# Performance work log

Measured on AMD Instinct MI355X. Metric: run time of the kernel, lower is better.

Reference implementation:

```python
import jax, jax.numpy as jnp
import numpy as np

D_MODEL = 1024
NUM_HEADS = 16
HEAD_DIM = D_MODEL // NUM_HEADS
B, S = 4, 2048


def setup_inputs() -> dict:
    key = jax.random.key(0)
    ks = jax.random.split(key, 12)
    s = 1.0 / np.sqrt(D_MODEL)
    return {
        "inputs_q": jax.random.normal(ks[0], (B, S, D_MODEL), jnp.float32),
        "inputs_k": jax.random.normal(ks[1], (B, S, D_MODEL), jnp.float32),
        "inputs_v": jax.random.normal(ks[2], (B, S, D_MODEL), jnp.float32),
        "Wq": jax.random.normal(ks[3], (D_MODEL, D_MODEL), jnp.float32) * s,
        "bq": jax.random.normal(ks[4], (D_MODEL,), jnp.float32) * 0.01,
        "Wk": jax.random.normal(ks[5], (D_MODEL, D_MODEL), jnp.float32) * s,
        "bk": jax.random.normal(ks[6], (D_MODEL,), jnp.float32) * 0.01,
        "Wv": jax.random.normal(ks[7], (D_MODEL, D_MODEL), jnp.float32) * s,
        "bv": jax.random.normal(ks[8], (D_MODEL,), jnp.float32) * 0.01,
        "Wo": jax.random.normal(ks[9], (D_MODEL, D_MODEL), jnp.float32) * s,
        "bo": jax.random.normal(ks[10], (D_MODEL,), jnp.float32) * 0.01,
    }


def reference(inputs_q, inputs_k, inputs_v, Wq, bq, Wk, bk, Wv, bv, Wo, bo):
    b, s, _ = inputs_q.shape
    # linear projections
    q = inputs_q @ Wq + bq  # [b, s, d_model]
    k = inputs_k @ Wk + bk
    v = inputs_v @ Wv + bv
    # split heads: bsd -> bhsd
    q = q.reshape(b, s, NUM_HEADS, HEAD_DIM).transpose(0, 2, 1, 3)
    k = k.reshape(b, s, NUM_HEADS, HEAD_DIM).transpose(0, 2, 1, 3)
    v = v.reshape(b, s, NUM_HEADS, HEAD_DIM).transpose(0, 2, 1, 3)
    scale = 1.0 / jnp.sqrt(jnp.asarray(HEAD_DIM, q.dtype))
    scores = jnp.einsum('bhqd,bhkd->bhqk', q, k) * scale  # [b,h,s,s]
    # causal mask: position q attends to k <= q
    causal = jnp.tril(jnp.ones((s, s), dtype=bool))
    scores = jnp.where(causal[None, None], scores, jnp.asarray(-jnp.inf, scores.dtype))
    attn = jax.nn.softmax(scores, axis=-1)
    ctx = jnp.einsum('bhqk,bhkd->bhqd', attn, v)  # [b,h,s,hd]
    ctx = ctx.transpose(0, 2, 1, 3).reshape(b, s, D_MODEL)
    return ctx @ Wo + bo
```

## Files before the change

kernel.cpp:

```cpp
#include <hip/hip_runtime.h>
#include <math.h>
#include <type_traits>

typedef __bf16 bf16;
typedef __attribute__((ext_vector_type(8))) __bf16 bf16x8;
typedef __attribute__((ext_vector_type(4))) float f32x4;
typedef __attribute__((ext_vector_type(16))) float f32x16;

#define SEQ 2048
#define DM 1024
#define NH 16
#define HD 64
#define BATCH 4

#define NEG_BIG (-1e30f)
#define SCALE_L2E 0.18033688011f

__device__ inline bf16x8 cvt_f32x8(const float* p) {
  f32x4 x0 = *(const f32x4*)p;
  f32x4 x1 = *(const f32x4*)(p + 4);
  bf16x8 r;
  r[0] = (bf16)x0[0]; r[1] = (bf16)x0[1]; r[2] = (bf16)x0[2]; r[3] = (bf16)x0[3];
  r[4] = (bf16)x1[0]; r[5] = (bf16)x1[1]; r[6] = (bf16)x1[2]; r[7] = (bf16)x1[3];
  return r;
}

__device__ inline void async_copy16(const bf16* g, bf16* l) {
  __builtin_amdgcn_global_load_lds(
      (const __attribute__((address_space(1))) unsigned int*)g,
      (__attribute__((address_space(3))) unsigned int*)l, 16, 0, 0);
}

__global__ __launch_bounds__(256) void cvt_kernel(const float* __restrict__ src,
                                                  bf16* __restrict__ dst) {
  size_t i = ((size_t)blockIdx.x * 256 + threadIdx.x) * 8;
  *(bf16x8*)(dst + i) = cvt_f32x8(src + i);
}

__global__ __launch_bounds__(256) void transpose_w_kernel(
    const float* __restrict__ Wq, const float* __restrict__ Wk,
    const float* __restrict__ Wv, const float* __restrict__ Wo,
    bf16* __restrict__ Tq, bf16* __restrict__ Tk,
    bf16* __restrict__ Tv, bf16* __restrict__ To) {
  __shared__ bf16 tile[64 * 66];
  int z = blockIdx.z;
  const float* src = (z == 0) ? Wq : (z == 1) ? Wk : (z == 2) ? Wv : Wo;
  bf16* dst = (z == 0) ? Tq : (z == 1) ? Tk : (z == 2) ? Tv : To;
  int n0 = blockIdx.x * 64, k0 = blockIdx.y * 64;
  int t = threadIdx.x;
  int c = t & 63, rr = t >> 6;
#pragma unroll
  for (int i = 0; i < 16; i++) {
    int k = i * 4 + rr;
    tile[k * 66 + c] = (bf16)src[(size_t)(k0 + k) * DM + n0 + c];
  }
  __syncthreads();
#pragma unroll
  for (int i = 0; i < 16; i++) {
    int n = i * 4 + rr;
    dst[(size_t)(n0 + n) * DM + k0 + c] = tile[c * 66 + n];
  }
}

template <typename CT, int MODE>
__global__ __launch_bounds__(256) void gemm_bias_kernel(
    const bf16* __restrict__ A, const bf16* __restrict__ Bt,
    const float* __restrict__ bias, CT* __restrict__ C) {
  __shared__ bf16 As[2][128 * 32];
  __shared__ bf16 Bs[2][128 * 32];
  int m0 = blockIdx.x * 128, n0 = blockIdx.y * 128;
  int t = threadIdx.x;
  int wave = t >> 6, lane = t & 63, lr = lane & 15, lq = lane >> 4;
  int wm = (wave & 1) * 64, wn = (wave >> 1) * 64;

  f32x4 acc[4][4];
#pragma unroll
  for (int i = 0; i < 4; i++)
#pragma unroll
    for (int j = 0; j < 4; j++) acc[i][j] = (f32x4){0.f, 0.f, 0.f, 0.f};

  int srow = wave * 32 + (lane >> 2);
  int skc = lane & 3;
  const bf16* gA0 = A + (size_t)(m0 + srow) * DM + skc * 8;
  const bf16* gA1 = gA0 + (size_t)16 * DM;
  const bf16* gB0 = Bt + (size_t)(n0 + srow) * DM + skc * 8;
  const bf16* gB1 = gB0 + (size_t)16 * DM;
  int oA0 = (wave * 128) * 8;
  int oA1 = (wave * 128 + 64) * 8;

  auto stage = [&](int buf) {
    async_copy16(gA0, &As[buf][oA0]);
    async_copy16(gA1, &As[buf][oA1]);
    async_copy16(gB0, &Bs[buf][oA0]);
    async_copy16(gB1, &Bs[buf][oA1]);
    gA0 += 32; gA1 += 32; gB0 += 32; gB1 += 32;
  };

  stage(0);
  __syncthreads();
  int cur = 0;
  for (int k0 = 0; k0 < DM; k0 += 32) {
    if (k0 + 32 < DM) stage(cur ^ 1);

    bf16x8 af[4], bfr[4];
#pragma unroll
    for (int i = 0; i < 4; i++)
      af[i] = *(const bf16x8*)&As[cur][(wm + i * 16 + lr) * 32 + lq * 8];
#pragma unroll
    for (int j = 0; j < 4; j++)
      bfr[j] = *(const bf16x8*)&Bs[cur][(wn + j * 16 + lr) * 32 + lq * 8];
    __builtin_amdgcn_s_setprio(1);
#pragma unroll
    for (int i = 0; i < 4; i++)
#pragma unroll
      for (int j = 0; j < 4; j++)
        acc[i][j] = __builtin_amdgcn_mfma_f32_16x16x32_bf16(af[i], bfr[j],
                                                            acc[i][j], 0, 0, 0);
    __builtin_amdgcn_s_setprio(0);
    __syncthreads();
    cur ^= 1;
  }

#pragma unroll
  for (int j = 0; j < 4; j++) {
    int col = n0 + wn + j * 16 + lr;
    float bv = bias[col];
#pragma unroll
    for (int i = 0; i < 4; i++) {
      int row0 = m0 + wm + i * 16 + lq * 4;
#pragma unroll
      for (int r = 0; r < 4; r++) {
        int row = row0 + r;
        float v = acc[i][j][r] + bv;
        if constexpr (MODE == 0) {
          C[(size_t)row * DM + col] = (CT)v;
        } else if constexpr (MODE == 1) {
          int b = row >> 11, s = row & 2047, h = col >> 6, d = col & 63;
          C[((size_t)(b * NH + h) * SEQ + s) * HD + d] = (CT)v;
        } else {
          int b = row >> 11, s = row & 2047, h = col >> 6, d = col & 63;
          C[((size_t)(b * NH + h) * HD + d) * SEQ + s] = (CT)v;
        }
      }
    }
  }
}

__global__ __launch_bounds__(256, 2) void attention_kernel(
    const bf16* __restrict__ Qc, const bf16* __restrict__ Kc,
    const bf16* __restrict__ Vt, bf16* __restrict__ ctx) {
  int t = threadIdx.x, wave = t >> 6, lane = t & 63;
  int l31 = lane & 31, hh = lane >> 5;

  int bid = blockIdx.x;
  int xcd = bid & 7, qq = bid >> 3;
  int g = xcd + 8 * (qq & 7);
  int bx = qq >> 3;
  int h = g & 15, b = g >> 4;
  int p = bx * 4 + wave;

  const bf16* Qb = Qc + (size_t)(b * NH + h) * SEQ * HD;
  const bf16* Kb = Kc + (size_t)(b * NH + h) * SEQ * HD;
  const bf16* Vb = Vt + (size_t)(b * NH + h) * HD * SEQ;
  bf16* Cb = ctx + (size_t)b * SEQ * DM + h * HD;

#pragma unroll 1
  for (int pass = 0; pass < 2; pass++) {
    int tq = pass ? (63 - p) : p;
    int q0 = tq * 32;

    bf16x8 qf[4];
#pragma unroll
    for (int st = 0; st < 4; st++)
      qf[st] = *(const bf16x8*)&Qb[(size_t)(q0 + l31) * HD + st * 16 + hh * 8];

    f32x16 o[2];
#pragma unroll
    for (int dt = 0; dt < 2; dt++)
#pragma unroll
      for (int r = 0; r < 16; r++) o[dt][r] = 0.f;
    float m_st = NEG_BIG, l_st = 0.f;

    int nch = (tq >> 1) + 1;
#pragma unroll 1
    for (int c = 0; c < nch; c++) {
      int kv0 = c * 64;
      bf16x8 kf[2][4];
#pragma unroll
      for (int kt = 0; kt < 2; kt++)
#pragma unroll
        for (int st = 0; st < 4; st++)
          kf[kt][st] = *(const bf16x8*)&Kb[(size_t)(kv0 + kt * 32 + l31) * HD +
                                           st * 16 + hh * 8];
      bf16x8 vf[2][4];
#pragma unroll
      for (int dt = 0; dt < 2; dt++)
#pragma unroll
        for (int ks = 0; ks < 4; ks++)
          vf[dt][ks] = *(const bf16x8*)&Vb[(size_t)(dt * 32 + l31) * SEQ + kv0 +
                                           ks * 16 + hh * 8];

      f32x16 s[2];
      __builtin_amdgcn_s_setprio(1);
#pragma unroll
      for (int kt = 0; kt < 2; kt++) {
        f32x16 acc;
#pragma unroll
        for (int r = 0; r < 16; r++) acc[r] = 0.f;
#pragma unroll
        for (int st = 0; st < 4; st++)
          acc = __builtin_amdgcn_mfma_f32_32x32x16_bf16(kf[kt][st], qf[st],
                                                        acc, 0, 0, 0);
        s[kt] = acc;
      }
      __builtin_amdgcn_s_setprio(0);

      bool diag = (c == nch - 1);
      if (diag) {
        int q_g = q0 + l31;
#pragma unroll
        for (int kt = 0; kt < 2; kt++)
#pragma unroll
          for (int r = 0; r < 16; r++) {
            int key = kv0 + kt * 32 + (r & 3) + 8 * (r >> 2) + 4 * hh;
            float v = s[kt][r] * SCALE_L2E;
            s[kt][r] = (key > q_g) ? NEG_BIG : v;
          }
      } else {
#pragma unroll
        for (int kt = 0; kt < 2; kt++)
#pragma unroll
          for (int r = 0; r < 16; r++) s[kt][r] *= SCALE_L2E;
      }

      float mx = s[0][0];
#pragma unroll
      for (int r = 1; r < 16; r++) mx = fmaxf(mx, s[0][r]);
#pragma unroll
      for (int r = 0; r < 16; r++) mx = fmaxf(mx, s[1][r]);
      mx = fmaxf(mx, __shfl_xor(mx, 32));
      float mnew = fmaxf(m_st, mx);
      float alpha = exp2f(m_st - mnew);
      m_st = mnew;
      float rs = 0.f;
#pragma unroll
      for (int kt = 0; kt < 2; kt++)
#pragma unroll
        for (int r = 0; r < 16; r++) {
          float pv = exp2f(s[kt][r] - mnew);
          s[kt][r] = pv;
          rs += pv;
        }
      rs += __shfl_xor(rs, 32);
      l_st = l_st * alpha + rs;
#pragma unroll
      for (int dt = 0; dt < 2; dt++)
#pragma unroll
        for (int r = 0; r < 16; r++) o[dt][r] *= alpha;

      unsigned int W[2][8];
#pragma unroll
      for (int kt = 0; kt < 2; kt++)
#pragma unroll
        for (int w = 0; w < 8; w++) {
          unsigned int u;
          asm("v_cvt_pk_bf16_f32 %0, %1, %2"
              : "=v"(u)
              : "v"(s[kt][2 * w]), "v"(s[kt][2 * w + 1]));
          W[kt][w] = u;
        }
      bf16x8 pf[4];
#pragma unroll
      for (int kt = 0; kt < 2; kt++) {
        unsigned int x1 = hh ? W[kt][0] : W[kt][2];
        unsigned int x2 = hh ? W[kt][1] : W[kt][3];
        unsigned int x3 = hh ? W[kt][4] : W[kt][6];
        unsigned int x4 = hh ? W[kt][5] : W[kt][7];
        unsigned int y1 = (unsigned int)__shfl_xor((int)x1, 32);
        unsigned int y2 = (unsigned int)__shfl_xor((int)x2, 32);
        unsigned int y3 = (unsigned int)__shfl_xor((int)x3, 32);
        unsigned int y4 = (unsigned int)__shfl_xor((int)x4, 32);
        unsigned int* f0 = (unsigned int*)&pf[2 * kt];
        unsigned int* f1 = (unsigned int*)&pf[2 * kt + 1];
        f0[0] = hh ? y1 : W[kt][0];
        f0[1] = hh ? y2 : W[kt][1];
        f0[2] = hh ? W[kt][2] : y1;
        f0[3] = hh ? W[kt][3] : y2;
        f1[0] = hh ? y3 : W[kt][4];
        f1[1] = hh ? y4 : W[kt][5];
        f1[2] = hh ? W[kt][6] : y3;
        f1[3] = hh ? W[kt][7] : y4;
      }

      __builtin_amdgcn_s_setprio(1);
#pragma unroll
      for (int dt = 0; dt < 2; dt++)
#pragma unroll
        for (int ks = 0; ks < 4; ks++)
          o[dt] = __builtin_amdgcn_mfma_f32_32x32x16_bf16(vf[dt][ks], pf[ks],
                                                          o[dt], 0, 0, 0);
      __builtin_amdgcn_s_setprio(0);
    }

    float inv = 1.f / l_st;
    int row = q0 + l31;
#pragma unroll
    for (int dt = 0; dt < 2; dt++)
#pragma unroll
      for (int r = 0; r < 16; r += 2) {
        float va = o[dt][r] * inv;
        float vb = o[dt][r + 1] * inv;
        unsigned int u;
        asm("v_cvt_pk_bf16_f32 %0, %1, %2" : "=v"(u) : "v"(va), "v"(vb));
        int d = dt * 32 + (r & 3) + 8 * (r >> 2) + 4 * hh;
        *(unsigned int*)&Cb[(size_t)row * DM + d] = u;
      }
  }
}

extern "C" void kernel_launch(void* const* d_in, const int* in_sizes, int n_in,
                              void* d_out, int out_size, void* d_ws,
                              size_t ws_size, hipStream_t stream) {
  const float* iq = (const float*)d_in[0];
  const float* ik = (const float*)d_in[1];
  const float* iv = (const float*)d_in[2];
  const float* Wq = (const float*)d_in[3];
  const float* bq = (const float*)d_in[4];
  const float* Wk = (const float*)d_in[5];
  const float* bk = (const float*)d_in[6];
  const float* Wv = (const float*)d_in[7];
  const float* bv = (const float*)d_in[8];
  const float* Wo = (const float*)d_in[9];
  const float* bo = (const float*)d_in[10];

  char* ws = (char*)d_ws;
  const size_t MB = 1024 * 1024;
  bf16* Tq = (bf16*)(ws + 0 * MB);
  bf16* Tk = (bf16*)(ws + 2 * MB);
  bf16* Tv = (bf16*)(ws + 4 * MB);
  bf16* To = (bf16*)(ws + 6 * MB);
  bf16* Qc = (bf16*)(ws + 8 * MB);
  bf16* Kc = (bf16*)(ws + 24 * MB);
  bf16* X = (bf16*)(ws + 40 * MB);
  bf16* Vtp = (bf16*)d_out;
  bf16* Cx = (bf16*)(ws + 40 * MB);

  transpose_w_kernel<<<dim3(16, 16, 4), 256, 0, stream>>>(Wq, Wk, Wv, Wo, Tq,
                                                          Tk, Tv, To);
  cvt_kernel<<<dim3(4096), 256, 0, stream>>>(iq, X);
  gemm_bias_kernel<bf16, 1><<<dim3(64, 8), 256, 0, stream>>>(X, Tq, bq, Qc);
  cvt_kernel<<<dim3(4096), 256, 0, stream>>>(ik, X);
  gemm_bias_kernel<bf16, 1><<<dim3(64, 8), 256, 0, stream>>>(X, Tk, bk, Kc);
  cvt_kernel<<<dim3(4096), 256, 0, stream>>>(iv, X);
  gemm_bias_kernel<bf16, 2><<<dim3(64, 8), 256, 0, stream>>>(X, Tv, bv, Vtp);
  attention_kernel<<<dim3(512), 256, 0, stream>>>(Qc, Kc, Vtp, Cx);
  gemm_bias_kernel<float, 0><<<dim3(64, 8), 256, 0, stream>>>(Cx, To, bo,
                                                              (float*)d_out);
}
```

Baseline: 395.6 us.

## Fuse fp32-to-bf16 input conversion into batched QKV projection GEMM

Removes the three separate conversion kernels and instead loads fp32 activations straight into registers inside the GEMM, converting to bf16 before writing to shared memory. The three Q/K/V projections are batched into one launch using a z grid dimension. This is meant to cut the extra global round-trip of the bf16 copy, remove five launches, and give more blocks per launch to fill the GPU. The trade-off is that A-tile loads become synchronous register loads doubled in bytes rather than async LDS copies, which adds register pressure and latency to hide.

```diff
diff --git a/kernel.cpp b/kernel.cpp
--- a/kernel.cpp
+++ b/kernel.cpp
@@ -16,9 +16,7 @@
 #define NEG_BIG (-1e30f)
 #define SCALE_L2E 0.18033688011f
 
-__device__ inline bf16x8 cvt_f32x8(const float* p) {
-  f32x4 x0 = *(const f32x4*)p;
-  f32x4 x1 = *(const f32x4*)(p + 4);
+__device__ inline bf16x8 pack_bf16x8(f32x4 x0, f32x4 x1) {
   bf16x8 r;
   r[0] = (bf16)x0[0]; r[1] = (bf16)x0[1]; r[2] = (bf16)x0[2]; r[3] = (bf16)x0[3];
   r[4] = (bf16)x1[0]; r[5] = (bf16)x1[1]; r[6] = (bf16)x1[2]; r[7] = (bf16)x1[3];
@@ -29,12 +27,6 @@
   __builtin_amdgcn_global_load_lds(
       (const __attribute__((address_space(1))) unsigned int*)g,
       (__attribute__((address_space(3))) unsigned int*)l, 16, 0, 0);
-}
-
-__global__ __launch_bounds__(256) void cvt_kernel(const float* __restrict__ src,
-                                                  bf16* __restrict__ dst) {
-  size_t i = ((size_t)blockIdx.x * 256 + threadIdx.x) * 8;
-  *(bf16x8*)(dst + i) = cvt_f32x8(src + i);
 }
 
 __global__ __launch_bounds__(256) void transpose_w_kernel(
@@ -62,6 +54,117 @@
   }
 }
 
+__global__ __launch_bounds__(256) void qkv_gemm_kernel(
+    const float* __restrict__ Aq, const float* __restrict__ Ak,
+    const float* __restrict__ Av, const bf16* __restrict__ Tq,
+    const bf16* __restrict__ Tk, const bf16* __restrict__ Tv,
+    const float* __restrict__ bq, const float* __restrict__ bk,
+    const float* __restrict__ bv, bf16* __restrict__ Cq,
+    bf16* __restrict__ Ck, bf16* __restrict__ Cv) {
+  int z = blockIdx.z;
+  const float* A = (z == 0) ? Aq : (z == 1) ? Ak : Av;
+  const bf16* Bt = (z == 0) ? Tq : (z == 1) ? Tk : Tv;
+  const float* bias = (z == 0) ? bq : (z == 1) ? bk : bv;
+  bf16* C = (z == 0) ? Cq : (z == 1) ? Ck : Cv;
+
+  __shared__ bf16 As[2][128 * 32];
+  __shared__ bf16 Bs[2][128 * 32];
+  int m0 = blockIdx.x * 128, n0 = blockIdx.y * 128;
+  int t = threadIdx.x;
+  int wave = t >> 6, lane = t & 63, lr = lane & 15, lq = lane >> 4;
+  int wm = (wave & 1) * 64, wn = (wave >> 1) * 64;
+
+  f32x4 acc[4][4];
+#pragma unroll
+  for (int i = 0; i < 4; i++)
+#pragma unroll
+    for (int j = 0; j < 4; j++) acc[i][j] = (f32x4){0.f, 0.f, 0.f, 0.f};
+
+  int arow = t >> 2;
+  int acolf = (t & 3) * 8;
+  const float* gA = A + (size_t)(m0 + arow) * DM + acolf;
+  const float* gA2 = gA + (size_t)64 * DM;
+  f32x4 ar[2][2];
+
+  auto loadA = [&](int k0) {
+    ar[0][0] = *(const f32x4*)(gA + k0);
+    ar[0][1] = *(const f32x4*)(gA + k0 + 4);
+    ar[1][0] = *(const f32x4*)(gA2 + k0);
+    ar[1][1] = *(const f32x4*)(gA2 + k0 + 4);
+  };
+  auto cvtwriteA = [&](int buf) {
+    *(bf16x8*)&As[buf][arow * 32 + acolf] = pack_bf16x8(ar[0][0], ar[0][1]);
+    *(bf16x8*)&As[buf][(arow + 64) * 32 + acolf] =
+        pack_bf16x8(ar[1][0], ar[1][1]);
+  };
+
+  int srow = wave * 32 + (lane >> 2);
+  int skc = lane & 3;
+  const bf16* gB0 = Bt + (size_t)(n0 + srow) * DM + skc * 8;
+  const bf16* gB1 = gB0 + (size_t)16 * DM;
+  int oB0 = (wave * 128) * 8;
+  int oB1 = (wave * 128 + 64) * 8;
+  auto stageB = [&](int buf) {
+    async_copy16(gB0, &Bs[buf][oB0]);
+    async_copy16(gB1, &Bs[buf][oB1]);
+    gB0 += 32; gB1 += 32;
+  };
+
+  loadA(0);
+  stageB(0);
+  cvtwriteA(0);
+  __syncthreads();
+
+  int cur = 0;
+  for (int k0 = 0; k0 < DM; k0 += 32) {
+    bool more = (k0 + 32 < DM);
+    if (more) {
+      loadA(k0 + 32);
+      stageB(cur ^ 1);
+    }
+
+    bf16x8 af[4], bfr[4];
+#pragma unroll
+    for (int i = 0; i < 4; i++)
+      af[i] = *(const bf16x8*)&As[cur][(wm + i * 16 + lr) * 32 + lq * 8];
+#pragma unroll
+    for (int j = 0; j < 4; j++)
+      bfr[j] = *(const bf16x8*)&Bs[cur][(wn + j * 16 + lr) * 32 + lq * 8];
+    __builtin_amdgcn_s_setprio(1);
+#pragma unroll
+    for (int i = 0; i < 4; i++)
+#pragma unroll
+      for (int j = 0; j < 4; j++)
+        acc[i][j] = __builtin_amdgcn_mfma_f32_16x16x32_bf16(af[i], bfr[j],
+                                                            acc[i][j], 0, 0, 0);
+    __builtin_amdgcn_s_setprio(0);
+    if (more) cvtwriteA(cur ^ 1);
+    __syncthreads();
+    cur ^= 1;
+  }
+
+#pragma unroll
+  for (int j = 0; j < 4; j++) {
+    int col = n0 + wn + j * 16 + lr;
+    float bv2 = bias[col];
+#pragma unroll
+    for (int i = 0; i < 4; i++) {
+      int row0 = m0 + wm + i * 16 + lq * 4;
+#pragma unroll
+      for (int r = 0; r < 4; r++) {
+        int row = row0 + r;
+        float v = acc[i][j][r] + bv2;
+        int b = row >> 11, s = row & 2047, h = col >> 6, d = col & 63;
+        if (z < 2) {
+          C[((size_t)(b * NH + h) * SEQ + s) * HD + d] = (bf16)v;
+        } else {
+          C[((size_t)(b * NH + h) * HD + d) * SEQ + s] = (bf16)v;
+        }
+      }
+    }
+  }
+}
+
 template <typename CT, int MODE>
 __global__ __launch_bounds__(256) void gemm_bias_kernel(
     const bf16* __restrict__ A, const bf16* __restrict__ Bt,
@@ -134,12 +237,9 @@
         float v = acc[i][j][r] + bv;
         if constexpr (MODE == 0) {
           C[(size_t)row * DM + col] = (CT)v;
-        } else if constexpr (MODE == 1) {
+        } else {
           int b = row >> 11, s = row & 2047, h = col >> 6, d = col & 63;
           C[((size_t)(b * NH + h) * SEQ + s) * HD + d] = (CT)v;
-        } else {
-          int b = row >> 11, s = row & 2047, h = col >> 6, d = col & 63;
-          C[((size_t)(b * NH + h) * HD + d) * SEQ + s] = (CT)v;
         }
       }
     }
@@ -341,18 +441,13 @@
   bf16* To = (bf16*)(ws + 6 * MB);
   bf16* Qc = (bf16*)(ws + 8 * MB);
   bf16* Kc = (bf16*)(ws + 24 * MB);
-  bf16* X = (bf16*)(ws + 40 * MB);
+  bf16* Cx = (bf16*)(ws + 40 * MB);
   bf16* Vtp = (bf16*)d_out;
-  bf16* Cx = (bf16*)(ws + 40 * MB);
 
   transpose_w_kernel<<<dim3(16, 16, 4), 256, 0, stream>>>(Wq, Wk, Wv, Wo, Tq,
                                                           Tk, Tv, To);
-  cvt_kernel<<<dim3(4096), 256, 0, stream>>>(iq, X);
-  gemm_bias_kernel<bf16, 1><<<dim3(64, 8), 256, 0, stream>>>(X, Tq, bq, Qc);
-  cvt_kernel<<<dim3(4096), 256, 0, stream>>>(ik, X);
-  gemm_bias_kernel<bf16, 1><<<dim3(64, 8), 256, 0, stream>>>(X, Tk, bk, Kc);
-  cvt_kernel<<<dim3(4096), 256, 0, stream>>>(iv, X);
-  gemm_bias_kernel<bf16, 2><<<dim3(64, 8), 256, 0, stream>>>(X, Tv, bv, Vtp);
+  qkv_gemm_kernel<<<dim3(64, 8, 3), 256, 0, stream>>>(
+      iq, ik, iv, Tq, Tk, Tv, bq, bk, bv, Qc, Kc, Vtp);
   attention_kernel<<<dim3(512), 256, 0, stream>>>(Qc, Kc, Vtp, Cx);
   gemm_bias_kernel<float, 0><<<dim3(64, 8), 256, 0, stream>>>(Cx, To, bo,
                                                               (float*)d_out);
```

New measurement: 405.4 us. +2.5%, slower.
